# Kernel tuning notes

Hardware: AMD Instinct MI355X
Metric: run time of the kernel (lower is better)

Reference implementation:

```python
import jax, jax.numpy as jnp
import numpy as np

N_NODES = 100000
N_EDGES = 3200000
NEG_SLOPE = 0.2  # PyG GATConv default


def _gat_conv(x, src, dst, W, a_src, a_dst, b, num_nodes):
    # x: [N, Fin]; src/dst: [E'] (self-loops already appended)
    h = x @ W                                   # [N, Fout]
    alpha_src = h @ a_src                       # [N]
    alpha_dst = h @ a_dst                       # [N]
    e = jax.nn.leaky_relu(alpha_src[src] + alpha_dst[dst], NEG_SLOPE)  # [E']
    # segment softmax over incoming edges of each destination node
    e_max = jax.ops.segment_max(e, dst, num_segments=num_nodes)
    e_exp = jnp.exp(e - e_max[dst])
    denom = jax.ops.segment_sum(e_exp, dst, num_segments=num_nodes)
    alpha = e_exp / (denom[dst] + 1e-16)        # [E']
    out = jax.ops.segment_sum(h[src] * alpha[:, None], dst, num_segments=num_nodes)
    return out + b


def setup_inputs() -> dict:
    key = jax.random.key(0)
    ks = jax.random.split(key, 10)
    x = jax.random.normal(ks[0], (N_NODES, 1), jnp.float32)
    edge_index = jax.random.randint(ks[1], (2, N_EDGES), 0, N_NODES, dtype=jnp.int64)
    s1 = 1.0  # glorot-ish scales
    return {
        "x": x,
        "edge_index": edge_index,
        "W1": jax.random.normal(ks[2], (1, 20), jnp.float32) * s1,
        "a_src1": jax.random.normal(ks[3], (20,), jnp.float32) * 0.3,
        "a_dst1": jax.random.normal(ks[4], (20,), jnp.float32) * 0.3,
        "b1": jnp.zeros((20,), jnp.float32),
        "W2": jax.random.normal(ks[5], (20, 20), jnp.float32) * (1.0 / np.sqrt(20.0)),
        "a_src2": jax.random.normal(ks[6], (20,), jnp.float32) * 0.3,
        "a_dst2": jax.random.normal(ks[7], (20,), jnp.float32) * 0.3,
        "b2": jnp.zeros((20,), jnp.float32),
        "Wl": jax.random.normal(ks[8], (20, 1), jnp.float32) * (1.0 / np.sqrt(20.0)),
        "bl": jnp.zeros((1,), jnp.float32),
    }


def reference(x, edge_index, W1, a_src1, a_dst1, b1, W2, a_src2, a_dst2, b2, Wl, bl):
    n = x.shape[0]
    loop = jnp.arange(n, dtype=edge_index.dtype)
    src = jnp.concatenate([edge_index[0], loop])  # add_self_loops=True
    dst = jnp.concatenate([edge_index[1], loop])
    h = _gat_conv(x, src, dst, W1, a_src1, a_dst1, b1, n)
    h = jax.nn.relu(h)
    h = _gat_conv(h, src, dst, W2, a_src2, a_dst2, b2, n)
    h = jax.nn.relu(h)
    return h @ Wl + bl  # [N, 1]
```

## Files before the change

### kernel.cpp

```cpp
#include <hip/hip_runtime.h>
#include <hip/hip_fp16.h>

#define FDIM 20
#define NSLOPE 0.2f
#define BSHIFT 7
#define BSIZE 128
#define BCAP 4800
#define MAXBUCK 800
#define PGRID 256
#define HSTRIDE 32
#define ABLK 512
#define ITMAX 13
#define CHCAP 12544
#define OFFSTRIDE 132

__device__ __forceinline__ float lrelu(float v) { return v > 0.f ? v : NSLOPE * v; }

__global__ void k_init(const float* __restrict__ x, const float* __restrict__ W1,
                       const float* __restrict__ a_src, const float* __restrict__ a_dst,
                       float2* __restrict__ PX, float* __restrict__ AD,
                       int* __restrict__ gcur, int N)
{
    int i = blockIdx.x * blockDim.x + threadIdx.x;
    if (i < MAXBUCK) gcur[i] = 0;
    if (i >= N) return;
    float cs = 0.f, cd = 0.f;
#pragma unroll
    for (int f = 0; f < FDIM; ++f) { float w = W1[f]; cs += w * a_src[f]; cd += w * a_dst[f]; }
    float xv = x[i];
    PX[i] = make_float2(xv * cs, xv);
    AD[i] = xv * cd;
}

__global__ void __launch_bounds__(1024)
k_part(const int* __restrict__ ei, int E, int nbuck,
       int* __restrict__ gcur, int* __restrict__ slab)
{
    __shared__ int hist[MAXBUCK];
    __shared__ int lofs[MAXBUCK];
    __shared__ int gbase[MAXBUCK];
    __shared__ int sbuf[CHCAP];
    __shared__ unsigned short sbk[CHCAP];
    const int tid = threadIdx.x;
    const int chunk = (E + PGRID - 1) / PGRID;
    const int c0 = blockIdx.x * chunk;
    const int c1 = min(c0 + chunk, E);
    for (int t = tid; t < nbuck; t += 1024) hist[t] = 0;
    __syncthreads();

    int ent[ITMAX], meta[ITMAX];
#pragma unroll
    for (int it = 0; it < ITMAX; ++it) {
        int i = c0 + tid + (it << 10);
        meta[it] = -1;
        if (i < c1) {
            int s = ei[i], d = ei[E + i];
            int b = d >> BSHIFT;
            int lp = atomicAdd(&hist[b], 1);
            ent[it]  = (s << BSHIFT) | (d & (BSIZE - 1));
            meta[it] = (lp << 10) | b;
        }
    }
    __syncthreads();

    int myc = 0;
    if (tid < nbuck) {
        myc = hist[tid];
        lofs[tid] = myc;
        gbase[tid] = myc ? atomicAdd(gcur + tid, myc) : 0;
    }
    __syncthreads();
    for (int o = 1; o < nbuck; o <<= 1) {
        int v = 0;
        if (tid < nbuck && tid >= o) v = lofs[tid - o];
        __syncthreads();
        if (tid < nbuck && tid >= o) lofs[tid] += v;
        __syncthreads();
    }
    if (tid < nbuck) lofs[tid] -= myc;
    __syncthreads();

#pragma unroll
    for (int it = 0; it < ITMAX; ++it) {
        int m = meta[it];
        if (m >= 0) {
            int b  = m & 1023;
            int lp = m >> 10;
            int pos = lofs[b] + lp;
            sbuf[pos] = ent[it];
            sbk[pos]  = (unsigned short)b;
        }
    }
    __syncthreads();

    const int cnt = c1 - c0;
    for (int i = tid; i < cnt; i += 1024) {
        int b  = sbk[i];
        int gp = gbase[b] + (i - lofs[b]);
        if (gp < BCAP) slab[(size_t)b * BCAP + gp] = sbuf[i];
    }
}

__device__ __forceinline__ void sort_bucket(const int* __restrict__ sp, int cnt,
                                            int* __restrict__ sedge,
                                            int* __restrict__ off,
                                            int* __restrict__ cur)
{
    const int tid = threadIdx.x;
    if (tid < BSIZE + 1) off[tid] = 0;
    __syncthreads();
    for (int i = tid; i < cnt; i += blockDim.x)
        atomicAdd(&off[(sp[i] & (BSIZE - 1)) + 1], 1);
    __syncthreads();
    for (int o = 1; o < BSIZE; o <<= 1) {
        int v = 0;
        if (tid < BSIZE && tid + 1 > o) v = off[tid + 1 - o];
        __syncthreads();
        if (tid < BSIZE) off[tid + 1] += v;
        __syncthreads();
    }
    if (tid < BSIZE) cur[tid] = off[tid];
    __syncthreads();
    for (int i = tid; i < cnt; i += blockDim.x) {
        int e = sp[i];
        int pos = atomicAdd(&cur[e & (BSIZE - 1)], 1);
        sedge[pos] = e >> BSHIFT;
    }
    __syncthreads();
}

__global__ void __launch_bounds__(ABLK)
k_agg1(const int* __restrict__ gcur, const int* __restrict__ slab,
       const float2* __restrict__ PX, const float* __restrict__ AD,
       const float* __restrict__ W1, const float* __restrict__ b1,
       const float* __restrict__ W2,
       const float* __restrict__ as2w, const float* __restrict__ ad2w,
       __half* __restrict__ H, float* __restrict__ AD2,
       int* __restrict__ sedge_g, int* __restrict__ off_g, int N)
{
    __shared__ int sedge[BCAP];
    __shared__ int off[BSIZE + 1], cur[BSIZE];
    __shared__ float sAD[BSIZE];
    __shared__ float sW1[FDIM], sb1[FDIM], sW2[FDIM * FDIM], sas[FDIM], sad[FDIM];
    const int tid = threadIdx.x;
    const int b = blockIdx.x;
    const int dbase = b << BSHIFT;
    if (tid < BSIZE) { int d = dbase + tid; sAD[tid] = (d < N) ? AD[d] : 0.f; }
    for (int t = tid; t < FDIM * FDIM; t += ABLK) sW2[t] = W2[t];
    if (tid >= 480 && tid < 480 + FDIM) {
        int k = tid - 480;
        sW1[k] = W1[k]; sb1[k] = b1[k]; sas[k] = as2w[k]; sad[k] = ad2w[k];
    }
    const int cnt = min(gcur[b], BCAP);
    sort_bucket(slab + (size_t)b * BCAP, cnt, sedge, off, cur);

    for (int i = tid; i < cnt; i += ABLK) sedge_g[(size_t)b * BCAP + i] = sedge[i];
    if (tid <= BSIZE) off_g[b * OFFSTRIDE + tid] = off[tid];

    const int dl = tid >> 2, sub = tid & 3;
    const float adv = sAD[dl];
    float den = 0.f, sx = 0.f;
    const int e1 = off[dl + 1];
#pragma unroll 2
    for (int j = off[dl] + sub; j < e1; j += 4) {
        int s = sedge[j];
        float2 p = PX[s];
        float w = __expf(lrelu(p.x + adv));
        den += w; sx += w * p.y;
    }
    den += __shfl_xor(den, 1); den += __shfl_xor(den, 2);
    sx  += __shfl_xor(sx, 1);  sx  += __shfl_xor(sx, 2);
    const int d = dbase + dl;
    if (sub == 0 && d < N) {
        float2 p = PX[d];
        float w = __expf(lrelu(p.x + adv));
        den += w; sx += w * p.y;
        float sv = sx / (den + 1e-16f);
        float tk[FDIM];
#pragma unroll
        for (int k = 0; k < FDIM; ++k) {
            float tv = sv * sW1[k] + sb1[k];
            tk[k] = tv > 0.f ? tv : 0.f;
        }
        float pas = 0.f, pad = 0.f;
        __half2* hrow = (__half2*)(H + (size_t)d * HSTRIDE);
#pragma unroll
        for (int f = 0; f < FDIM; f += 2) {
            float h0 = 0.f, h1 = 0.f;
#pragma unroll
            for (int k = 0; k < FDIM; ++k) {
                h0 += tk[k] * sW2[k * FDIM + f];
                h1 += tk[k] * sW2[k * FDIM + f + 1];
            }
            hrow[f >> 1] = __halves2half2(__float2half(h0), __float2half(h1));
            pas += h0 * sas[f] + h1 * sas[f + 1];
            pad += h0 * sad[f] + h1 * sad[f + 1];
        }
        *(float*)(H + (size_t)d * HSTRIDE + FDIM) = pas;
        AD2[d] = pad;
    }
}

__global__ void __launch_bounds__(ABLK)
k_agg2(const int* __restrict__ gcur, const int* __restrict__ sedge_g,
       const int* __restrict__ off_g,
       const __half* __restrict__ H, const float* __restrict__ AD2,
       const float* __restrict__ b2, const float* __restrict__ Wl,
       const float* __restrict__ bl,
       float* __restrict__ out, int N)
{
    __shared__ int sedge[BCAP];
    __shared__ int off[BSIZE + 1];
    __shared__ float sAD[BSIZE];
    __shared__ float sb2[FDIM], sWl[FDIM];
    const int tid = threadIdx.x;
    const int b = blockIdx.x;
    const int dbase = b << BSHIFT;
    if (tid < BSIZE) { int d = dbase + tid; sAD[tid] = (d < N) ? AD2[d] : 0.f; }
    if (tid >= 480 && tid < 480 + FDIM) {
        int k = tid - 480;
        sb2[k] = b2[k]; sWl[k] = Wl[k];
    }
    const int cnt = min(gcur[b], BCAP);
    for (int i = tid; i < cnt; i += ABLK) sedge[i] = sedge_g[(size_t)b * BCAP + i];
    if (tid <= BSIZE) off[tid] = off_g[b * OFFSTRIDE + tid];
    __syncthreads();

    const int dl = tid >> 2, sub = tid & 3;
    const float adv = sAD[dl];
    float den = 0.f;
    float acc[FDIM];
#pragma unroll
    for (int k = 0; k < FDIM; ++k) acc[k] = 0.f;
    const int e1 = off[dl + 1];
#pragma unroll 2
    for (int j = off[dl] + sub; j < e1; j += 4) {
        int s = sedge[j];
        const uint4* rp = (const uint4*)(H + (size_t)s * HSTRIDE);
        uint4 a = rp[0];
        uint4 bb = rp[1];
        uint4 c = rp[2];
        float w = __expf(lrelu(__uint_as_float(c.z) + adv));
        den += w;
        float2 f;
        f = __half22float2(*(__half2*)&a.x);  acc[0]  += w * f.x; acc[1]  += w * f.y;
        f = __half22float2(*(__half2*)&a.y);  acc[2]  += w * f.x; acc[3]  += w * f.y;
        f = __half22float2(*(__half2*)&a.z);  acc[4]  += w * f.x; acc[5]  += w * f.y;
        f = __half22float2(*(__half2*)&a.w);  acc[6]  += w * f.x; acc[7]  += w * f.y;
        f = __half22float2(*(__half2*)&bb.x); acc[8]  += w * f.x; acc[9]  += w * f.y;
        f = __half22float2(*(__half2*)&bb.y); acc[10] += w * f.x; acc[11] += w * f.y;
        f = __half22float2(*(__half2*)&bb.z); acc[12] += w * f.x; acc[13] += w * f.y;
        f = __half22float2(*(__half2*)&bb.w); acc[14] += w * f.x; acc[15] += w * f.y;
        f = __half22float2(*(__half2*)&c.x);  acc[16] += w * f.x; acc[17] += w * f.y;
        f = __half22float2(*(__half2*)&c.y);  acc[18] += w * f.x; acc[19] += w * f.y;
    }
    den += __shfl_xor(den, 1); den += __shfl_xor(den, 2);
#pragma unroll
    for (int k = 0; k < FDIM; ++k) {
        acc[k] += __shfl_xor(acc[k], 1);
        acc[k] += __shfl_xor(acc[k], 2);
    }
    const int d = dbase + dl;
    if (sub == 0 && d < N) {
        const uint4* rp = (const uint4*)(H + (size_t)d * HSTRIDE);
        uint4 a = rp[0], bb = rp[1], c = rp[2];
        float w = __expf(lrelu(__uint_as_float(c.z) + adv));
        den += w;
        float hv[FDIM];
        float2 f;
        f = __half22float2(*(__half2*)&a.x);  hv[0]  = f.x; hv[1]  = f.y;
        f = __half22float2(*(__half2*)&a.y);  hv[2]  = f.x; hv[3]  = f.y;
        f = __half22float2(*(__half2*)&a.z);  hv[4]  = f.x; hv[5]  = f.y;
        f = __half22float2(*(__half2*)&a.w);  hv[6]  = f.x; hv[7]  = f.y;
        f = __half22float2(*(__half2*)&bb.x); hv[8]  = f.x; hv[9]  = f.y;
        f = __half22float2(*(__half2*)&bb.y); hv[10] = f.x; hv[11] = f.y;
        f = __half22float2(*(__half2*)&bb.z); hv[12] = f.x; hv[13] = f.y;
        f = __half22float2(*(__half2*)&bb.w); hv[14] = f.x; hv[15] = f.y;
        f = __half22float2(*(__half2*)&c.x);  hv[16] = f.x; hv[17] = f.y;
        f = __half22float2(*(__half2*)&c.y);  hv[18] = f.x; hv[19] = f.y;
        float inv = 1.f / (den + 1e-16f);
        float r = 0.f;
#pragma unroll
        for (int k = 0; k < FDIM; ++k) {
            float v = (acc[k] + w * hv[k]) * inv + sb2[k];
            v = v > 0.f ? v : 0.f;
            r += v * sWl[k];
        }
        out[d] = r + bl[0];
    }
}

extern "C" void kernel_launch(void* const* d_in, const int* in_sizes, int n_in,
                              void* d_out, int out_size, void* d_ws, size_t ws_size,
                              hipStream_t stream)
{
    const float* x      = (const float*)d_in[0];
    const int*   ei     = (const int*)d_in[1];
    const float* W1     = (const float*)d_in[2];
    const float* a_src1 = (const float*)d_in[3];
    const float* a_dst1 = (const float*)d_in[4];
    const float* b1     = (const float*)d_in[5];
    const float* W2     = (const float*)d_in[6];
    const float* a_src2 = (const float*)d_in[7];
    const float* a_dst2 = (const float*)d_in[8];
    const float* b2     = (const float*)d_in[9];
    const float* Wl     = (const float*)d_in[10];
    const float* bl     = (const float*)d_in[11];
    float* out = (float*)d_out;

    const int N = in_sizes[0];
    const int E = in_sizes[1] / 2;
    const int NBUCK = (N + BSIZE - 1) >> BSHIFT;

    __half* H    = (__half*)d_ws;
    float2* PX   = (float2*)(H + (size_t)N * HSTRIDE);
    float*  AD   = (float*)(PX + N);
    float*  AD2  = AD + N;
    int*  gcur   = (int*)(AD2 + N);
    int*  slab   = gcur + MAXBUCK;
    int*  sedge_g = slab + (size_t)MAXBUCK * BCAP;
    int*  off_g   = sedge_g + (size_t)MAXBUCK * BCAP;

    const int nb_n = (N + 255) / 256;

    k_init<<<nb_n, 256, 0, stream>>>(x, W1, a_src1, a_dst1, PX, AD, gcur, N);
    k_part<<<PGRID, 1024, 0, stream>>>(ei, E, NBUCK, gcur, slab);
    k_agg1<<<NBUCK, ABLK, 0, stream>>>(gcur, slab, PX, AD, W1, b1, W2,
                                       a_src2, a_dst2, H, AD2, sedge_g, off_g, N);
    k_agg2<<<NBUCK, ABLK, 0, stream>>>(gcur, sedge_g, off_g, H, AD2, b2, Wl, bl, out, N);
}
```

Baseline: 185.0 us.

## Split feature dimension across lanes in layer-2 aggregation instead of edges

The layer-2 aggregation kernel now has each of the 4 lanes per destination load one 16-byte slice of the neighbor's feature row and loop over all edges, instead of each lane handling a quarter of the edges with full-row loads. The source attention scalar is moved to offset 24 so lane 3's slice carries it, and it is broadcast with a shuffle. This cuts per-thread accumulators from 20 to 8 and replaces the 20-way cross-lane reduction with a single scalar reduction of the final output. In exchange each lane runs four times as many loop iterations, each with a dependent shuffle, and lane 3 does mostly idle arithmetic.

```diff
diff --git a/kernel.cpp b/kernel.cpp
--- a/kernel.cpp
+++ b/kernel.cpp
@@ -196,7 +196,7 @@
             pas += h0 * sas[f] + h1 * sas[f + 1];
             pad += h0 * sad[f] + h1 * sad[f + 1];
         }
-        *(float*)(H + (size_t)d * HSTRIDE + FDIM) = pas;
+        *(float*)(H + (size_t)d * HSTRIDE + 24) = pas;
         AD2[d] = pad;
     }
 }
@@ -227,67 +227,55 @@
     __syncthreads();
 
     const int dl = tid >> 2, sub = tid & 3;
+    const int lane3 = (tid & 63) | 3;
     const float adv = sAD[dl];
     float den = 0.f;
-    float acc[FDIM];
-#pragma unroll
-    for (int k = 0; k < FDIM; ++k) acc[k] = 0.f;
+    float acc[8];
+#pragma unroll
+    for (int t = 0; t < 8; ++t) acc[t] = 0.f;
     const int e1 = off[dl + 1];
 #pragma unroll 2
-    for (int j = off[dl] + sub; j < e1; j += 4) {
+    for (int j = off[dl]; j < e1; ++j) {
         int s = sedge[j];
-        const uint4* rp = (const uint4*)(H + (size_t)s * HSTRIDE);
-        uint4 a = rp[0];
-        uint4 bb = rp[1];
-        uint4 c = rp[2];
-        float w = __expf(lrelu(__uint_as_float(c.z) + adv));
+        uint4 q = ((const uint4*)(H + (size_t)s * HSTRIDE))[sub];
+        float al = __shfl(__uint_as_float(q.x), lane3);
+        float w = __expf(lrelu(al + adv));
         den += w;
         float2 f;
-        f = __half22float2(*(__half2*)&a.x);  acc[0]  += w * f.x; acc[1]  += w * f.y;
-        f = __half22float2(*(__half2*)&a.y);  acc[2]  += w * f.x; acc[3]  += w * f.y;
-        f = __half22float2(*(__half2*)&a.z);  acc[4]  += w * f.x; acc[5]  += w * f.y;
-        f = __half22float2(*(__half2*)&a.w);  acc[6]  += w * f.x; acc[7]  += w * f.y;
-        f = __half22float2(*(__half2*)&bb.x); acc[8]  += w * f.x; acc[9]  += w * f.y;
-        f = __half22float2(*(__half2*)&bb.y); acc[10] += w * f.x; acc[11] += w * f.y;
-        f = __half22float2(*(__half2*)&bb.z); acc[12] += w * f.x; acc[13] += w * f.y;
-        f = __half22float2(*(__half2*)&bb.w); acc[14] += w * f.x; acc[15] += w * f.y;
-        f = __half22float2(*(__half2*)&c.x);  acc[16] += w * f.x; acc[17] += w * f.y;
-        f = __half22float2(*(__half2*)&c.y);  acc[18] += w * f.x; acc[19] += w * f.y;
-    }
-    den += __shfl_xor(den, 1); den += __shfl_xor(den, 2);
-#pragma unroll
-    for (int k = 0; k < FDIM; ++k) {
-        acc[k] += __shfl_xor(acc[k], 1);
-        acc[k] += __shfl_xor(acc[k], 2);
-    }
+        f = __half22float2(*(__half2*)&q.x); acc[0] += w * f.x; acc[1] += w * f.y;
+        f = __half22float2(*(__half2*)&q.y); acc[2] += w * f.x; acc[3] += w * f.y;
+        f = __half22float2(*(__half2*)&q.z); acc[4] += w * f.x; acc[5] += w * f.y;
+        f = __half22float2(*(__half2*)&q.w); acc[6] += w * f.x; acc[7] += w * f.y;
+    }
+
     const int d = dbase + dl;
-    if (sub == 0 && d < N) {
-        const uint4* rp = (const uint4*)(H + (size_t)d * HSTRIDE);
-        uint4 a = rp[0], bb = rp[1], c = rp[2];
-        float w = __expf(lrelu(__uint_as_float(c.z) + adv));
+    float r = 0.f;
+    if (d < N) {
+        uint4 q = ((const uint4*)(H + (size_t)d * HSTRIDE))[sub];
+        float al = __shfl(__uint_as_float(q.x), lane3);
+        float w = __expf(lrelu(al + adv));
         den += w;
-        float hv[FDIM];
+        float hv[8];
         float2 f;
-        f = __half22float2(*(__half2*)&a.x);  hv[0]  = f.x; hv[1]  = f.y;
-        f = __half22float2(*(__half2*)&a.y);  hv[2]  = f.x; hv[3]  = f.y;
-        f = __half22float2(*(__half2*)&a.z);  hv[4]  = f.x; hv[5]  = f.y;
-        f = __half22float2(*(__half2*)&a.w);  hv[6]  = f.x; hv[7]  = f.y;
-        f = __half22float2(*(__half2*)&bb.x); hv[8]  = f.x; hv[9]  = f.y;
-        f = __half22float2(*(__half2*)&bb.y); hv[10] = f.x; hv[11] = f.y;
-        f = __half22float2(*(__half2*)&bb.z); hv[12] = f.x; hv[13] = f.y;
-        f = __half22float2(*(__half2*)&bb.w); hv[14] = f.x; hv[15] = f.y;
-        f = __half22float2(*(__half2*)&c.x);  hv[16] = f.x; hv[17] = f.y;
-        f = __half22float2(*(__half2*)&c.y);  hv[18] = f.x; hv[19] = f.y;
+        f = __half22float2(*(__half2*)&q.x); hv[0] = f.x; hv[1] = f.y;
+        f = __half22float2(*(__half2*)&q.y); hv[2] = f.x; hv[3] = f.y;
+        f = __half22float2(*(__half2*)&q.z); hv[4] = f.x; hv[5] = f.y;
+        f = __half22float2(*(__half2*)&q.w); hv[6] = f.x; hv[7] = f.y;
         float inv = 1.f / (den + 1e-16f);
-        float r = 0.f;
-#pragma unroll
-        for (int k = 0; k < FDIM; ++k) {
-            float v = (acc[k] + w * hv[k]) * inv + sb2[k];
-            v = v > 0.f ? v : 0.f;
-            r += v * sWl[k];
-        }
-        out[d] = r + bl[0];
-    }
+        const int base = sub << 3;
+        const int nf = (sub < 2) ? 8 : (sub == 2 ? 4 : 0);
+#pragma unroll
+        for (int t = 0; t < 8; ++t) {
+            if (t < nf) {
+                float v = (acc[t] + w * hv[t]) * inv + sb2[base + t];
+                v = v > 0.f ? v : 0.f;
+                r += v * sWl[base + t];
+            }
+        }
+    }
+    r += __shfl_xor(r, 1);
+    r += __shfl_xor(r, 2);
+    if (sub == 0 && d < N) out[d] = r + bl[0];
 }
 
 extern "C" void kernel_launch(void* const* d_in, const int* in_sizes, int n_in,
```

New measurement: 181.8 us. About the same (-1.8%).
